# Optimization experiments

Hardware: AMD Instinct MI355X
Metric: run time of the kernel (lower is better)

Reference implementation:

```python
import jax, jax.numpy as jnp
import numpy as np

SEQ, HID, IN, THETA = 4096, 512, 512, 5


def setup_inputs() -> dict:
    key = jax.random.key(0)
    k0, k1, k2, k3, k4 = jax.random.split(key, 5)
    return {
        "input": jax.random.normal(k0, (1, SEQ, IN), jnp.float32),
        "internal": jax.random.normal(k1, (THETA + 1, SEQ, HID), jnp.float32) * 0.1,
        "state": jnp.zeros((1, 1, HID), jnp.float32),
        "W_ih": jax.random.normal(k2, (HID, IN), jnp.float32) / np.sqrt(IN).astype(np.float32),
        "W_hh": jax.random.normal(k3, (HID, HID), jnp.float32) / np.sqrt(HID).astype(np.float32),
        "b": jax.random.normal(k4, (HID,), jnp.float32) * 0.01,
        "theta": THETA,
    }


def reference(input, internal, state, W_ih, W_hh, b, theta):
    # Unbatched path (batched=False), continuousTheta=False, trunc >= seq (no detach).
    # Cell: h' = tanh(x @ W_ih.T + h @ W_hh.T + b + noise); out = h'.
    x = input[0]                      # [S, I]
    pre_x = x @ W_ih.T + b            # [S, H] precompute input drive
    h0 = state[0, 0]                  # [H]

    # Main recurrence over the sequence (theta index 0 of internal drives it).
    def step(h, px_n):
        px, n = px_n
        h_new = jnp.tanh(px + h @ W_hh.T + n)
        return h_new, h_new

    _, hs = jax.lax.scan(step, h0, (pre_x, internal[0]))   # hs: [S, H]

    # Theta rollouts: padded input is zero, so drive = b + noise. The rollout at
    # every timestep starts from that timestep's main state -> vectorize over S
    # and scan over the theta axis.
    def roll(H, n):
        H_new = jnp.tanh(b + H @ W_hh.T + n)
        return H_new, H_new

    _, Hs = jax.lax.scan(roll, hs, internal[1:])           # Hs: [theta, S, H]

    outputs = jnp.concatenate([hs[None], Hs], axis=0)      # [theta+1, S, H]
    final_state = hs[-1][None, None]                        # [1, 1, H]
    return outputs, final_state
```

## Files before the change

kernel.cpp:

```cpp
#include <hip/hip_runtime.h>
#include <cstdint>
#include <cstddef>

#define SEQ 4096
#define HID 512
#define NTHETA 5
#define NBLK 8
#define RPB 64
#define NMAIL 4
#define SENT_BITS 0x40000000u

typedef unsigned long long u64;

__device__ __forceinline__ float tanh_fast(float x) {
  x = fminf(fmaxf(x, -20.0f), 20.0f);
  const float e = __expf(2.0f * x);
  return (e - 1.0f) / (e + 1.0f);
}

__device__ __forceinline__ uint4 load_x4_sc1(const unsigned* p) {
  uint4 u;
  asm volatile("global_load_dwordx4 %0, %1, off sc1\n\ts_waitcnt vmcnt(0)"
               : "=v"(u) : "v"(p) : "memory");
  return u;
}

__device__ __forceinline__ bool has_sent(uint4 u) {
  return u.x == SENT_BITS || u.y == SENT_BITS ||
         u.z == SENT_BITS || u.w == SENT_BITS;
}

__device__ __forceinline__ uint4 poll_chunk(const unsigned* src,
                                            const unsigned* safe) {
  uint4 u = load_x4_sc1(src);
  int it = 0;
  while (has_sent(u)) {
    ++it;
    if ((it & 7) == 0) {
      const unsigned* s = (it >= 4096) ? safe : src;
      u.x = __hip_atomic_load(s + 0, __ATOMIC_RELAXED, __HIP_MEMORY_SCOPE_AGENT);
      u.y = __hip_atomic_load(s + 1, __ATOMIC_RELAXED, __HIP_MEMORY_SCOPE_AGENT);
      u.z = __hip_atomic_load(s + 2, __ATOMIC_RELAXED, __HIP_MEMORY_SCOPE_AGENT);
      u.w = __hip_atomic_load(s + 3, __ATOMIC_RELAXED, __HIP_MEMORY_SCOPE_AGENT);
    } else {
      u = load_x4_sc1(src);
    }
  }
  return u;
}

__device__ __forceinline__ float red16(float v) {
  int p;
  p = __builtin_amdgcn_update_dpp(0, __float_as_int(v), 0xB1, 0xF, 0xF, true);
  v += __int_as_float(p);
  p = __builtin_amdgcn_update_dpp(0, __float_as_int(v), 0x4E, 0xF, 0xF, true);
  v += __int_as_float(p);
  v += __int_as_float(__builtin_amdgcn_ds_swizzle(__float_as_int(v), 0x101F));
  p = __builtin_amdgcn_update_dpp(0, __float_as_int(v), 0x128, 0xF, 0xF, true);
  v += __int_as_float(p);
  return v;
}

__device__ __forceinline__ int swz(int f) {
  return (f & ~7) | ((f ^ (f >> 3)) & 7);
}

__global__ __launch_bounds__(256) void gemm_bias_noise(
    const float* __restrict__ A, const float* __restrict__ W,
    const float* __restrict__ bias, const float* __restrict__ noise,
    float* __restrict__ C, int K, int doTanh)
{
  const int N = HID;
  const int bm = blockIdx.y, bn = blockIdx.x;
  const int tid = threadIdx.x;
  const int tx = tid & 15, ty = tid >> 4;
  const int row0 = bm * 64, col0 = bn * 64;
  __shared__ float As[16][68];
  __shared__ float Ws[16][68];
  float acc[4][4] = {{0.f, 0.f, 0.f, 0.f}, {0.f, 0.f, 0.f, 0.f},
                     {0.f, 0.f, 0.f, 0.f}, {0.f, 0.f, 0.f, 0.f}};
  const int lrow = tid >> 2, lkq = tid & 3;
  for (int kt = 0; kt < K; kt += 16) {
    const float4 av = *(const float4*)&A[(size_t)(row0 + lrow) * K + kt + lkq * 4];
    const float4 wv = *(const float4*)&W[(size_t)(col0 + lrow) * K + kt + lkq * 4];
    __syncthreads();
    As[lkq * 4 + 0][lrow] = av.x; As[lkq * 4 + 1][lrow] = av.y;
    As[lkq * 4 + 2][lrow] = av.z; As[lkq * 4 + 3][lrow] = av.w;
    Ws[lkq * 4 + 0][lrow] = wv.x; Ws[lkq * 4 + 1][lrow] = wv.y;
    Ws[lkq * 4 + 2][lrow] = wv.z; Ws[lkq * 4 + 3][lrow] = wv.w;
    __syncthreads();
#pragma unroll
    for (int k = 0; k < 16; ++k) {
      const float4 a = *(const float4*)&As[k][ty * 4];
      const float4 bq = *(const float4*)&Ws[k][tx * 4];
      const float a4[4] = {a.x, a.y, a.z, a.w};
      const float b4[4] = {bq.x, bq.y, bq.z, bq.w};
#pragma unroll
      for (int i = 0; i < 4; ++i)
#pragma unroll
        for (int j = 0; j < 4; ++j)
          acc[i][j] = fmaf(a4[i], b4[j], acc[i][j]);
    }
  }
  const float4 bv = *(const float4*)&bias[col0 + tx * 4];
#pragma unroll
  for (int i = 0; i < 4; ++i) {
    const int row = row0 + ty * 4 + i;
    const float4 nv = *(const float4*)&noise[(size_t)row * N + col0 + tx * 4];
    float4 o;
    o.x = acc[i][0] + bv.x + nv.x;
    o.y = acc[i][1] + bv.y + nv.y;
    o.z = acc[i][2] + bv.z + nv.z;
    o.w = acc[i][3] + bv.w + nv.w;
    if (doTanh) {
      o.x = tanh_fast(o.x); o.y = tanh_fast(o.y);
      o.z = tanh_fast(o.z); o.w = tanh_fast(o.w);
    }
    *(float4*)&C[(size_t)row * N + col0 + tx * 4] = o;
  }
}

__global__ void fill_sentinel(uint4* __restrict__ p, int n4) {
  const int i = blockIdx.x * blockDim.x + threadIdx.x;
  if (i < n4) p[i] = make_uint4(SENT_BITS, SENT_BITS, SENT_BITS, SENT_BITS);
}

__global__ __launch_bounds__(512, 2) void recurrence(
    const float* __restrict__ Whh, const float* __restrict__ drive,
    const float* __restrict__ h0, unsigned* __restrict__ plane0,
    unsigned* __restrict__ mail)
{
  const size_t PL = (size_t)SEQ * HID;
  const int blk = blockIdx.x;
  const int base = blk * RPB;
  const int tid = threadIdx.x;
  const int i = tid >> 4;
  const int j = tid & 15;
  const int r0 = base + 2 * i;

  __shared__ __align__(16) float hbuf[2][HID];

  float w0[32], w1[32];
  {
    const volatile float* p0 = &Whh[(size_t)r0 * HID + 32 * j];
    const volatile float* p1 = p0 + HID;
#pragma unroll
    for (int c = 0; c < 32; ++c) { w0[c] = p0[c]; w1[c] = p1[c]; }
  }

  const int ch = (tid < blk * 16) ? tid : tid + 16;
  const int wslot = swz(ch);
  const int z0 = swz(r0 >> 2) * 4 + (r0 & 3);
  unsigned* mymail = mail + (size_t)(blk & 3) * PL;

  hbuf[0][swz(tid >> 2) * 4 + (tid & 3)] = h0[tid];

  for (int t = 0; t < SEQ; ++t) {
    const int buf = t & 1;

    float2 dr = make_float2(0.f, 0.f);
    if (j == 0) dr = *(const float2*)&drive[(size_t)t * HID + r0];

    if (t > 0 && tid < 112) {
      const unsigned* src  = &mymail[(size_t)(t - 1) * HID + 4 * ch];
      const unsigned* safe = &plane0[(size_t)(t - 1) * HID + 4 * ch];
      const uint4 u = poll_chunk(src, safe);
      ((uint4*)hbuf[buf])[wslot] = u;
    }
    __syncthreads();
    asm volatile("" :: "v"(dr.x), "v"(dr.y));

    float a00 = 0.f, a01 = 0.f, a02 = 0.f, a03 = 0.f;
    float a10 = 0.f, a11 = 0.f, a12 = 0.f, a13 = 0.f;
#pragma unroll
    for (int c = 0; c < 8; ++c) {
      const float4 h4 = *(const float4*)&hbuf[buf][(8 * j + ((c ^ j) & 7)) * 4];
      a00 = fmaf(w0[4 * c + 0], h4.x, a00);
      a01 = fmaf(w0[4 * c + 1], h4.y, a01);
      a02 = fmaf(w0[4 * c + 2], h4.z, a02);
      a03 = fmaf(w0[4 * c + 3], h4.w, a03);
      a10 = fmaf(w1[4 * c + 0], h4.x, a10);
      a11 = fmaf(w1[4 * c + 1], h4.y, a11);
      a12 = fmaf(w1[4 * c + 2], h4.z, a12);
      a13 = fmaf(w1[4 * c + 3], h4.w, a13);
    }
    float s0 = red16((a00 + a01) + (a02 + a03));
    float s1 = red16((a10 + a11) + (a12 + a13));

    if (j == 0) {
      const float y0 = tanh_fast(s0 + dr.x);
      const float y1 = tanh_fast(s1 + dr.y);
      const u64 pk = (u64)__float_as_uint(y0) | ((u64)__float_as_uint(y1) << 32);
      const size_t off = (size_t)t * HID + r0;
#pragma unroll
      for (int m = 0; m < NMAIL; ++m)
        __hip_atomic_store((u64*)&mail[m * PL + off], pk,
                           __ATOMIC_RELAXED, __HIP_MEMORY_SCOPE_AGENT);
      __hip_atomic_store((u64*)&plane0[off], pk,
                         __ATOMIC_RELAXED, __HIP_MEMORY_SCOPE_AGENT);
      *(float2*)&hbuf[buf ^ 1][z0] = make_float2(y0, y1);
    }
  }
}

__global__ void copy_final(const float* __restrict__ src, float* __restrict__ dst) {
  dst[threadIdx.x] = src[threadIdx.x];
}

extern "C" void kernel_launch(void* const* d_in, const int* in_sizes, int n_in,
                              void* d_out, int out_size, void* d_ws, size_t ws_size,
                              hipStream_t stream) {
  const float* input    = (const float*)d_in[0];
  const float* internal = (const float*)d_in[1];
  const float* state    = (const float*)d_in[2];
  const float* W_ih     = (const float*)d_in[3];
  const float* W_hh     = (const float*)d_in[4];
  const float* bias     = (const float*)d_in[5];
  float* out = (float*)d_out;

  const size_t plane = (size_t)SEQ * HID;
  unsigned* plane0 = (unsigned*)out;
  unsigned* mail   = (unsigned*)(out + plane);
  float*    drive  = out + 5 * plane;

  fill_sentinel<<<((int)(5 * plane / 4) + 255) / 256, 256, 0, stream>>>(
      (uint4*)out, (int)(5 * plane / 4));

  dim3 gg(HID / 64, SEQ / 64);
  gemm_bias_noise<<<gg, 256, 0, stream>>>(input, W_ih, bias, internal, drive,
                                          HID, 0);
  recurrence<<<NBLK, 512, 0, stream>>>(W_hh, drive, state, plane0, mail);
  for (int k = 0; k < NTHETA; ++k) {
    gemm_bias_noise<<<gg, 256, 0, stream>>>(out + (size_t)k * plane, W_hh, bias,
                                            internal + (size_t)(k + 1) * plane,
                                            out + (size_t)(k + 1) * plane,
                                            HID, 1);
  }
  copy_final<<<1, HID, 0, stream>>>(out + (size_t)4095 * HID, out + 6 * plane);
}
```

Baseline: 6.197 ms.

## Split recurrence across 4 blocks of 128 rows with per-block mailboxes

Halves the number of cooperating workgroups in the sequential recurrence from 8 to 4, with each thread now holding four W_hh rows (128 weight registers) instead of two. Each block polls only the 384 hidden values produced by the other three blocks. Each block now has its own mailbox plane and writes only to the other blocks' mailboxes, dropping the shared 2-blocks-per-mailbox scheme. The aim is to cut cross-block communication and per-step polling latency on the critical path, at the cost of twice the FMA work per thread per step and higher register pressure.

```diff
diff --git a/kernel.cpp b/kernel.cpp
--- a/kernel.cpp
+++ b/kernel.cpp
@@ -5,9 +5,8 @@
 #define SEQ 4096
 #define HID 512
 #define NTHETA 5
-#define NBLK 8
-#define RPB 64
-#define NMAIL 4
+#define NBLK 4
+#define RPB 128
 #define SENT_BITS 0x40000000u
 
 typedef unsigned long long u64;
@@ -136,42 +135,48 @@
   const int tid = threadIdx.x;
   const int i = tid >> 4;
   const int j = tid & 15;
-  const int r0 = base + 2 * i;
+  const int r0 = base + 4 * i;
 
   __shared__ __align__(16) float hbuf[2][HID];
 
-  float w0[32], w1[32];
+  float w0[32], w1[32], w2[32], w3[32];
   {
     const volatile float* p0 = &Whh[(size_t)r0 * HID + 32 * j];
-    const volatile float* p1 = p0 + HID;
-#pragma unroll
-    for (int c = 0; c < 32; ++c) { w0[c] = p0[c]; w1[c] = p1[c]; }
-  }
-
-  const int ch = (tid < blk * 16) ? tid : tid + 16;
+#pragma unroll
+    for (int c = 0; c < 32; ++c) {
+      w0[c] = p0[c];
+      w1[c] = p0[c + HID];
+      w2[c] = p0[c + 2 * HID];
+      w3[c] = p0[c + 3 * HID];
+    }
+  }
+
+  const int ch = (tid < blk * 32) ? tid : tid + 32;
   const int wslot = swz(ch);
-  const int z0 = swz(r0 >> 2) * 4 + (r0 & 3);
-  unsigned* mymail = mail + (size_t)(blk & 3) * PL;
+  const int z0 = swz(r0 >> 2) * 4;
+  const unsigned* mymail = mail + (size_t)blk * PL;
 
   hbuf[0][swz(tid >> 2) * 4 + (tid & 3)] = h0[tid];
 
   for (int t = 0; t < SEQ; ++t) {
     const int buf = t & 1;
 
-    float2 dr = make_float2(0.f, 0.f);
-    if (j == 0) dr = *(const float2*)&drive[(size_t)t * HID + r0];
-
-    if (t > 0 && tid < 112) {
+    float4 dr = make_float4(0.f, 0.f, 0.f, 0.f);
+    if (j == 0) dr = *(const float4*)&drive[(size_t)t * HID + r0];
+
+    if (t > 0 && tid < 96) {
       const unsigned* src  = &mymail[(size_t)(t - 1) * HID + 4 * ch];
       const unsigned* safe = &plane0[(size_t)(t - 1) * HID + 4 * ch];
       const uint4 u = poll_chunk(src, safe);
       ((uint4*)hbuf[buf])[wslot] = u;
     }
     __syncthreads();
-    asm volatile("" :: "v"(dr.x), "v"(dr.y));
+    asm volatile("" :: "v"(dr.x), "v"(dr.y), "v"(dr.z), "v"(dr.w));
 
     float a00 = 0.f, a01 = 0.f, a02 = 0.f, a03 = 0.f;
     float a10 = 0.f, a11 = 0.f, a12 = 0.f, a13 = 0.f;
+    float a20 = 0.f, a21 = 0.f, a22 = 0.f, a23 = 0.f;
+    float a30 = 0.f, a31 = 0.f, a32 = 0.f, a33 = 0.f;
 #pragma unroll
     for (int c = 0; c < 8; ++c) {
       const float4 h4 = *(const float4*)&hbuf[buf][(8 * j + ((c ^ j) & 7)) * 4];
@@ -183,22 +188,45 @@
       a11 = fmaf(w1[4 * c + 1], h4.y, a11);
       a12 = fmaf(w1[4 * c + 2], h4.z, a12);
       a13 = fmaf(w1[4 * c + 3], h4.w, a13);
-    }
-    float s0 = red16((a00 + a01) + (a02 + a03));
-    float s1 = red16((a10 + a11) + (a12 + a13));
+      a20 = fmaf(w2[4 * c + 0], h4.x, a20);
+      a21 = fmaf(w2[4 * c + 1], h4.y, a21);
+      a22 = fmaf(w2[4 * c + 2], h4.z, a22);
+      a23 = fmaf(w2[4 * c + 3], h4.w, a23);
+      a30 = fmaf(w3[4 * c + 0], h4.x, a30);
+      a31 = fmaf(w3[4 * c + 1], h4.y, a31);
+      a32 = fmaf(w3[4 * c + 2], h4.z, a32);
+      a33 = fmaf(w3[4 * c + 3], h4.w, a33);
+    }
+    const float s0 = red16((a00 + a01) + (a02 + a03));
+    const float s1 = red16((a10 + a11) + (a12 + a13));
+    const float s2 = red16((a20 + a21) + (a22 + a23));
+    const float s3 = red16((a30 + a31) + (a32 + a33));
 
     if (j == 0) {
-      const float y0 = tanh_fast(s0 + dr.x);
-      const float y1 = tanh_fast(s1 + dr.y);
-      const u64 pk = (u64)__float_as_uint(y0) | ((u64)__float_as_uint(y1) << 32);
+      float4 y;
+      y.x = tanh_fast(s0 + dr.x);
+      y.y = tanh_fast(s1 + dr.y);
+      y.z = tanh_fast(s2 + dr.z);
+      y.w = tanh_fast(s3 + dr.w);
+      const u64 lo = (u64)__float_as_uint(y.x) | ((u64)__float_as_uint(y.y) << 32);
+      const u64 hi = (u64)__float_as_uint(y.z) | ((u64)__float_as_uint(y.w) << 32);
       const size_t off = (size_t)t * HID + r0;
 #pragma unroll
-      for (int m = 0; m < NMAIL; ++m)
-        __hip_atomic_store((u64*)&mail[m * PL + off], pk,
-                           __ATOMIC_RELAXED, __HIP_MEMORY_SCOPE_AGENT);
-      __hip_atomic_store((u64*)&plane0[off], pk,
-                         __ATOMIC_RELAXED, __HIP_MEMORY_SCOPE_AGENT);
-      *(float2*)&hbuf[buf ^ 1][z0] = make_float2(y0, y1);
+      for (int c = 0; c < NBLK; ++c) {
+        if (c != blk) {
+          u64* d = (u64*)&mail[(size_t)c * PL + off];
+          __hip_atomic_store(d + 0, lo, __ATOMIC_RELAXED,
+                             __HIP_MEMORY_SCOPE_AGENT);
+          __hip_atomic_store(d + 1, hi, __ATOMIC_RELAXED,
+                             __HIP_MEMORY_SCOPE_AGENT);
+        }
+      }
+      u64* d0 = (u64*)&plane0[off];
+      __hip_atomic_store(d0 + 0, lo, __ATOMIC_RELAXED,
+                         __HIP_MEMORY_SCOPE_AGENT);
+      __hip_atomic_store(d0 + 1, hi, __ATOMIC_RELAXED,
+                         __HIP_MEMORY_SCOPE_AGENT);
+      *(float4*)&hbuf[buf ^ 1][z0] = y;
     }
   }
 }
```

After: 7.332 ms. 1.18x slower.
